# Kernel optimization log

Hardware: AMD Instinct MI355X
Metric: run time of the kernel (lower is better)

Reference implementation:

```python
import jax, jax.numpy as jnp
import numpy as np

B, C, L = 8, 256, 2048      # batch, res_channels, seq_len
E = 2 * C                    # attention / S4 width = 512
CH = 4                       # S4 channels
SQRT_HALF = 0.7071067811865476


def setup_inputs() -> dict:
    key = jax.random.key(0)
    ks = jax.random.split(key, 12)
    def n(k, s, sc):
        return jax.random.normal(k, s, dtype=jnp.float32) * sc
    return dict(
        x=jax.random.normal(ks[0], (B, C, L), dtype=jnp.float32),
        original=jax.random.normal(ks[1], (B, C, L), dtype=jnp.float32),
        sn_scale=jnp.ones((1, C, 1), jnp.float32),
        conv_w=n(ks[2], (E, C, 3), 0.05), conv_b=jnp.zeros((E,), jnp.float32),
        s4_ln_g=jnp.ones((E,), jnp.float32), s4_ln_b=jnp.zeros((E,), jnp.float32),
        s4_kernel=n(ks[3], (CH, E, L), 0.01),           # long-conv kernel per channel
        s4_D=n(ks[4], (CH, E), 1.0),                     # skip connection D
        s4_out_w=n(ks[5], (E, CH * E), 0.02), s4_out_b=jnp.zeros((E,), jnp.float32),
        attn_v_w=n(ks[6], (E, E), 0.02), attn_v_b=jnp.zeros((E,), jnp.float32),
        attn_o_w=n(ks[7], (E, E), 0.02), attn_o_b=jnp.zeros((E,), jnp.float32),
        res_w=n(ks[8], (C, C, 1), 0.05), res_b=jnp.zeros((C,), jnp.float32),
        skip_w=n(ks[9], (C, C, 1), 0.05), skip_b=jnp.zeros((C,), jnp.float32),
    )


def reference(x, original, sn_scale, conv_w, conv_b, s4_ln_g, s4_ln_b,
              s4_kernel, s4_D, s4_out_w, s4_out_b,
              attn_v_w, attn_v_b, attn_o_w, attn_o_b,
              res_w, res_b, skip_w, skip_b):
    eps = 1e-8
    # RMSNorm over channel dim (dim=1)
    rms = jnp.sqrt(jnp.sum(x * x, axis=1, keepdims=True)) / np.sqrt(x.shape[1]).astype(np.float32)
    x_n = sn_scale * x / (rms + eps)
    # h = x + original (pre-norm x), conv k=3 pad=1, GELU
    h = x + original
    h = jax.lax.conv_general_dilated(h, conv_w, (1,), [(1, 1)],
                                     dimension_numbers=('NCH', 'OIH', 'NCH'))
    h = jax.nn.gelu(h + conv_b[None, :, None], approximate=False)
    # --- S4 / GConv: LN over channels, FFT causal long conv, D-skip, GELU, out linear ---
    mu = h.mean(axis=1, keepdims=True)
    var = h.var(axis=1, keepdims=True)
    u = (h - mu) / jnp.sqrt(var + 1e-5) * s4_ln_g[None, :, None] + s4_ln_b[None, :, None]
    n2 = 2 * u.shape[-1]
    uf = jnp.fft.rfft(u, n=n2)                      # (B, E, F)
    kf = jnp.fft.rfft(s4_kernel, n=n2)              # (CH, E, F)
    y = jnp.fft.irfft(jnp.einsum('bhf,chf->bchf', uf, kf), n=n2)[..., :u.shape[-1]]
    y = y + s4_D[None, :, :, None] * u[:, None]     # (B, CH, E, L)
    y = jax.nn.gelu(y.reshape(y.shape[0], CH * E, y.shape[-1]), approximate=False)
    h_t = jnp.einsum('oc,bcl->bol', s4_out_w, y) + s4_out_b[None, :, None]  # (B, E, L)
    # --- local-window MHA with window_size=1: each position attends only to itself,
    # softmax over a single unmasked score == 1, so out = Wo @ (Wv @ x + bv) + bo exactly ---
    v = jnp.einsum('oe,bel->bol', attn_v_w, h_t) + attn_v_b[None, :, None]
    h_s = jnp.einsum('oe,bel->bol', attn_o_w, v) + attn_o_b[None, :, None]
    h2 = h_t + h_s
    out = jnp.tanh(h2[:, :C]) * jax.nn.sigmoid(h2[:, C:])
    res = jnp.einsum('oc,bcl->bol', res_w[:, :, 0], out) + res_b[None, :, None]
    skip = jnp.einsum('oc,bcl->bol', skip_w[:, :, 0], out) + skip_b[None, :, None]
    return ((x_n + res) * SQRT_HALF, skip)
```

## Files before the change

kernel.cpp:

```cpp
#include <hip/hip_runtime.h>
#include <hip/hip_bf16.h>
#include <math.h>

typedef __attribute__((ext_vector_type(8))) short short8;
typedef __attribute__((ext_vector_type(4))) float float4_t;
typedef __attribute__((ext_vector_type(2))) float cf2;
typedef unsigned short ushort_t;
typedef unsigned int uint_t;

#define NBL 16384

#define WS_CONVA   ((size_t)0)
#define WS_WV      ((size_t)786432)
#define WS_WO      ((size_t)1310720)
#define WS_W1      ((size_t)1835008)
#define WS_WCAT    ((size_t)3932160)
#define WS_A2      ((size_t)4194304)
#define WS_ACOMB   ((size_t)4718592)
#define WS_BCOMB   ((size_t)6815744)
#define WS_XN      ((size_t)6819840)
#define WS_H0PT    ((size_t)23597056)
#define WS_U       ((size_t)31993856)
#define WS_GT      ((size_t)65548288)
#define WS_UF      WS_GT
#define WS_KF      ((size_t)99102720)
#define WS_G       ((size_t)132657152)
#define WS_GATET   (WS_G + 25165824)
#define WS_UB      ((size_t)208162816)

__device__ __forceinline__ float gelu_f(float x) {
    float t = x * x;
    float a2 = x * fmaf(0.07135481627f, t, 1.59576912161f);
    return x / (1.f + __expf(-a2));
}
__device__ __forceinline__ float tanh_f(float a) {
    return 1.f - 2.f / (1.f + __expf(2.f * a));
}
__device__ __forceinline__ float sigmoid_f(float b) {
    return 1.f / (1.f + __expf(-b));
}

__device__ __forceinline__ unsigned int pack_bf2(float a, float b) {
#if __has_builtin(__builtin_amdgcn_cvt_pk_bf16_f32)
    auto v = __builtin_amdgcn_cvt_pk_bf16_f32(a, b);
    unsigned int r; __builtin_memcpy(&r, &v, 4); return r;
#else
    __hip_bfloat16 ha = __float2bfloat16(a), hb = __float2bfloat16(b);
    unsigned short ua = *(unsigned short*)&ha, ub = *(unsigned short*)&hb;
    return (unsigned int)ua | ((unsigned int)ub << 16);
#endif
}
__device__ __forceinline__ ushort_t f2bfu(float a) {
    __hip_bfloat16 h = __float2bfloat16(a);
    return *(ushort_t*)&h;
}
__device__ __forceinline__ cf2 unpack_c(unsigned int v) {
    cf2 r;
    r.x = __uint_as_float(v << 16);
    r.y = __uint_as_float(v & 0xffff0000u);
    return r;
}
__device__ __forceinline__ float bf2f(ushort_t u) {
    return __uint_as_float(((unsigned int)u) << 16);
}

__device__ __forceinline__ void cp16(const ushort_t* g, ushort_t* l) {
    __builtin_amdgcn_global_load_lds(
        (__attribute__((address_space(1))) void*)(void*)g,
        (__attribute__((address_space(3))) void*)l, 16, 0, 0);
}

__device__ __forceinline__ cf2 cswap(cf2 a) { return __builtin_shufflevector(a, a, 1, 0); }
template<int SGN>
__device__ __forceinline__ cf2 cmuli(cf2 a) {
    cf2 s = cswap(a);
    return s * cf2{(float)(-SGN), (float)SGN};
}
__device__ __forceinline__ cf2 cmul(cf2 a, cf2 b) {
    cf2 t = cswap(a) * cf2{-b.y, b.y};
    return a * cf2{b.x, b.x} + t;
}
__device__ __forceinline__ cf2 cmulc(cf2 a, float wr, float wi) {
    cf2 t = cswap(a) * cf2{-wi, wi};
    return a * cf2{wr, wr} + t;
}

__global__ __launch_bounds__(256) void wprep_kernel(
    const float* __restrict__ conv_w, const float* __restrict__ attn_v_w,
    const float* __restrict__ attn_o_w, const float* __restrict__ s4_out_w,
    const float* __restrict__ res_w, const float* __restrict__ skip_w,
    __hip_bfloat16* __restrict__ convA, __hip_bfloat16* __restrict__ WvT,
    __hip_bfloat16* __restrict__ WoBf, __hip_bfloat16* __restrict__ W1T,
    __hip_bfloat16* __restrict__ Wcat)
{
    const int N0 = 393216, N1 = 655360, N2c = 917504, N3 = 1966080, N4 = 2097152;
    for (int i = blockIdx.x * 256 + threadIdx.x; i < N4; i += gridDim.x * 256) {
        if (i < N0) {
            int m = i / 768, r = i - m * 768, dk = r >> 8, c = r & 255;
            convA[i] = __float2bfloat16(conv_w[m * 768 + c * 3 + dk]);
        } else if (i < N1) {
            int j = i - N0; int row = j >> 9, e = j & 511;
            WvT[j] = __float2bfloat16(attn_v_w[e * 512 + row]);
        } else if (i < N2c) {
            WoBf[i - N1] = __float2bfloat16(attn_o_w[i - N1]);
        } else if (i < N3) {
            int j = i - N2c; int ck = j >> 9, e = j & 511;
            W1T[j] = __float2bfloat16(s4_out_w[e * 2048 + ck]);
        } else {
            int j = i - N3; int m = j >> 8, c = j & 255;
            float v = (m < 256) ? res_w[m * 256 + c] : skip_w[(m - 256) * 256 + c];
            Wcat[j] = __float2bfloat16(v);
        }
    }
}

__global__ __launch_bounds__(256) void bias2_kernel(
    const __hip_bfloat16* __restrict__ A2, const float* __restrict__ s4_out_b,
    const float* __restrict__ attn_o_w, const float* __restrict__ attn_v_b,
    const float* __restrict__ attn_o_b, float* __restrict__ bcomb)
{
    __shared__ float red[256];
    int o = blockIdx.x, t = threadIdx.x;
    float s = 0.f;
    for (int e = t; e < 512; e += 256)
        s += __bfloat162float(A2[o * 512 + e]) * s4_out_b[e] + attn_o_w[o * 512 + e] * attn_v_b[e];
    red[t] = s; __syncthreads();
    for (int k = 128; k > 0; k >>= 1) { if (t < k) red[t] += red[t + k]; __syncthreads(); }
    if (t == 0) bcomb[o] = red[0] + attn_o_b[o];
}

__global__ __launch_bounds__(512) void prep_kernel(
    const float* __restrict__ x, const float* __restrict__ orig,
    const float* __restrict__ sn, ushort_t* __restrict__ xnb, ushort_t* __restrict__ h0pT)
{
    __shared__ float red[8][64];
    __shared__ ushort_t T[256 * 66];
    int blk = blockIdx.x, t = threadIdx.x;
    int lane = t & 63, cg = t >> 6;
    int b = blk >> 5, l0 = (blk & 31) << 6;
    size_t basein = (size_t)b * 524288 + l0 + lane;
    float ss = 0.f;
    for (int c = cg; c < 256; c += 8) {
        size_t idx = basein + (size_t)c * 2048;
        float xv = x[idx], ov = orig[idx];
        ss += xv * xv;
        T[c * 66 + lane] = f2bfu(xv + ov);
    }
    red[cg][lane] = ss;
    __syncthreads();
    float tot = 0.f;
    #pragma unroll
    for (int k = 0; k < 8; ++k) tot += red[k][lane];
    float inv = 1.0f / (sqrtf(tot) * 0.0625f + 1e-8f);
    __hip_bfloat16* xo = (__hip_bfloat16*)xnb;
    for (int c = cg; c < 256; c += 8) {
        size_t idx = basein + (size_t)c * 2048;
        xo[idx] = __float2bfloat16(sn[c] * x[idx] * inv);
    }
    int c2 = t & 255, half = t >> 8;
    size_t rowbase = (size_t)(b * 2050 + 1 + l0);
    for (int r = half; r < 64; r += 2)
        h0pT[(rowbase + r) * 256 + c2] = T[c2 * 66 + r];
    if ((blk & 31) == 0) {
        if (t < 256) h0pT[(size_t)(b * 2050) * 256 + t] = 0;
        else         h0pT[(size_t)(b * 2050 + 2049) * 256 + (t - 256)] = 0;
    }
}

__global__ __launch_bounds__(512) void ln_kernel(
    const ushort_t* __restrict__ h, ushort_t* __restrict__ ub,
    const float* __restrict__ gam, const float* __restrict__ bet)
{
    __shared__ float r1[8][64], r2[8][64];
    int blk = blockIdx.x, t = threadIdx.x;
    int lane = t & 63, og = t >> 6;
    int n = (blk << 6) + lane;
    float s1 = 0.f, s2 = 0.f;
    for (int o = og; o < 512; o += 8) { float v = bf2f(h[(size_t)o * NBL + n]); s1 += v; s2 += v * v; }
    r1[og][lane] = s1; r2[og][lane] = s2;
    __syncthreads();
    float mu = 0.f, m2 = 0.f;
    #pragma unroll
    for (int k = 0; k < 8; ++k) { mu += r1[k][lane]; m2 += r2[k][lane]; }
    mu *= (1.f / 512.f); m2 *= (1.f / 512.f);
    float rstd = rsqrtf(m2 - mu * mu + 1e-5f);
    int b = n >> 11, l = n & 2047;
    size_t sbase = (size_t)(b >> 1) * 4096 + 2 * l + (b & 1);
    for (int o = og; o < 512; o += 8) {
        size_t idx = (size_t)o * NBL + n;
        ub[(size_t)o * 16384 + sbase] = f2bfu((bf2f(h[idx]) - mu) * rstd * gam[o] + bet[o]);
    }
}

#define PERM(m) ((((m) & 3) << 2) | ((m) >> 2))

template<int SGN>
__device__ __forceinline__ void dft4p(cf2& a0, cf2& a1, cf2& a2, cf2& a3) {
    cf2 t0 = a0 + a2, t1 = a0 - a2, t2 = a1 + a3, t3 = a1 - a3;
    cf2 j3 = cmuli<SGN>(t3);
    a0 = t0 + t2; a2 = t0 - t2;
    a1 = t1 + j3; a3 = t1 - j3;
}
template<int SGN>
__device__ __forceinline__ void dft4p_half(cf2& a0, cf2& a1, cf2& a2, cf2& a3) {
    cf2 u0 = a0, u1 = a1;
    cf2 j1 = cmuli<SGN>(u1);
    a0 = u0 + u1; a2 = u0 - u1;
    a1 = u0 + j1; a3 = u0 - j1;
}
template<int SGN>
__device__ __forceinline__ void dft4p_out01(cf2 a0, cf2 a1, cf2 a2, cf2 a3, cf2& o0, cf2& o1) {
    cf2 t0 = a0 + a2, t1 = a0 - a2, t2 = a1 + a3, t3 = a1 - a3;
    o0 = t0 + t2;
    o1 = t1 + cmuli<SGN>(t3);
}

template<int SGN>
__device__ __forceinline__ void dft16_stepB(cf2* x) {
    const float sg = (float)SGN;
    const float C16[10] = {1.f, 0.92387953f, 0.70710678f, 0.38268343f, 0.f,
                           -0.38268343f, -0.70710678f, -0.92387953f, -1.f, -0.92387953f};
    const float S16[10] = {0.f, 0.38268343f, 0.70710678f, 0.92387953f, 1.f,
                           0.92387953f, 0.70710678f, 0.38268343f, 0.f, -0.38268343f};
    #pragma unroll
    for (int s = 1; s < 4; ++s)
        #pragma unroll
        for (int r = 1; r < 4; ++r) {
            int e = s * r;
            x[4 * s + r] = cmulc(x[4 * s + r], C16[e], sg * S16[e]);
        }
}
template<int SGN>
__device__ __forceinline__ void dft16p(cf2* x) {
    #pragma unroll
    for (int r = 0; r < 4; ++r) dft4p<SGN>(x[r], x[4 + r], x[8 + r], x[12 + r]);
    dft16_stepB<SGN>(x);
    #pragma unroll
    for (int s = 0; s < 4; ++s) dft4p<SGN>(x[4 * s], x[4 * s + 1], x[4 * s + 2], x[4 * s + 3]);
}
template<int SGN>
__device__ __forceinline__ void dft16_halfin(cf2* x) {
    #pragma unroll
    for (int r = 0; r < 4; ++r) dft4p_half<SGN>(x[r], x[4 + r], x[8 + r], x[12 + r]);
    dft16_stepB<SGN>(x);
    #pragma unroll
    for (int s = 0; s < 4; ++s) dft4p<SGN>(x[4 * s], x[4 * s + 1], x[4 * s + 2], x[4 * s + 3]);
}
template<int SGN>
__device__ __forceinline__ void dft16_halfout(cf2* x, cf2* y) {
    #pragma unroll
    for (int r = 0; r < 4; ++r) dft4p<SGN>(x[r], x[4 + r], x[8 + r], x[12 + r]);
    dft16_stepB<SGN>(x);
    #pragma unroll
    for (int s = 0; s < 4; ++s)
        dft4p_out01<SGN>(x[4 * s], x[4 * s + 1], x[4 * s + 2], x[4 * s + 3], y[s], y[4 + s]);
}

template<int SGN>
__device__ __forceinline__ void tw_after(cf2* x, float p, float invQ) {
    float s1, c1; __sincosf((float)SGN * 6.283185307179586f * p * invQ, &s1, &c1);
    cf2 w1 = {c1, s1}, w = w1;
    #pragma unroll
    for (int m = 1; m < 16; ++m) { x[PERM(m)] = cmul(x[PERM(m)], w); w = cmul(w, w1); }
}
template<int SGN>
__device__ __forceinline__ void tw_before(cf2* x, float p, float invQ) {
    float s1, c1; __sincosf((float)SGN * 6.283185307179586f * p * invQ, &s1, &c1);
    cf2 w1 = {c1, s1}, w = w1;
    #pragma unroll
    for (int j = 1; j < 16; ++j) { x[j] = cmul(x[j], w); w = cmul(w, w1); }
}

__global__ __launch_bounds__(256) void fft_fwd_kernel(
    const ushort_t* __restrict__ ubf, const float* __restrict__ s4k,
    uint4* __restrict__ uf, uint4* __restrict__ kf)
{
    __shared__ cf2 S[4368];
    int wg = blockIdx.x, t = threadIdx.x;
    cf2 x[16];
    if (wg < 2048) {
        int bp = wg >> 9, e = wg & 511;
        const unsigned int* p0 = (const unsigned int*)ubf + (size_t)e * 8192 + (size_t)bp * 2048;
        #pragma unroll
        for (int j = 0; j < 8; ++j) x[j] = unpack_c(p0[j * 256 + t]);
    } else {
        const float* p0 = s4k + (size_t)(wg - 2048) * 2048;
        #pragma unroll
        for (int j = 0; j < 8; ++j) x[j] = cf2{p0[j * 256 + t], 0.f};
    }
    dft16_halfin<-1>(x);
    tw_after<-1>(x, (float)t, 1.f / 4096.f);
    int tb = 17 * (t >> 4) + (t & 15);
    #pragma unroll
    for (int m = 0; m < 16; ++m) S[tb + 273 * m] = x[PERM(m)];
    __syncthreads();
    int b2 = 273 * (t >> 4) + (t & 15);
    #pragma unroll
    for (int j = 0; j < 16; ++j) x[j] = S[b2 + 17 * j];
    dft16p<-1>(x);
    tw_after<-1>(x, (float)(t & 15), 1.f / 256.f);
    #pragma unroll
    for (int m = 0; m < 16; ++m) S[b2 + 17 * m] = x[PERM(m)];
    __syncthreads();
    int b3 = 273 * (t >> 4) + 17 * (t & 15);
    #pragma unroll
    for (int j = 0; j < 16; ++j) x[j] = S[b3 + j];
    dft16p<-1>(x);
    const float sc = (wg < 2048) ? 1.f : (1.f / 4096.f);
    uint4* dst = ((wg < 2048) ? (uf + (size_t)wg * 1024) : (kf + (size_t)(wg - 2048) * 1024)) + 4 * t;
    #pragma unroll
    for (int q = 0; q < 4; ++q) {
        uint4 o;
        cf2 v0 = x[PERM(4 * q)] * sc, v1 = x[PERM(4 * q + 1)] * sc;
        cf2 v2 = x[PERM(4 * q + 2)] * sc, v3 = x[PERM(4 * q + 3)] * sc;
        o.x = pack_bf2(v0.x, v0.y);
        o.y = pack_bf2(v1.x, v1.y);
        o.z = pack_bf2(v2.x, v2.y);
        o.w = pack_bf2(v3.x, v3.y);
        dst[q] = o;
    }
}

__global__ __launch_bounds__(256) void fft_inv_kernel(
    const uint4* __restrict__ uf, const uint4* __restrict__ kf,
    unsigned int* __restrict__ g2)
{
    __shared__ cf2 S[4368];
    int wg = blockIdx.x, t = threadIdx.x;
    int bp = wg >> 11, ch = (wg >> 9) & 3, e = wg & 511;
    const uint4* zr = uf + (size_t)(bp * 512 + e) * 1024 + 4 * t;
    const uint4* kr = kf + (size_t)(ch * 512 + e) * 1024 + 4 * t;
    cf2 x[16];
    #pragma unroll
    for (int q = 0; q < 4; ++q) {
        uint4 a4 = zr[q], b4 = kr[q];
        x[4 * q + 0] = cmul(unpack_c(a4.x), unpack_c(b4.x));
        x[4 * q + 1] = cmul(unpack_c(a4.y), unpack_c(b4.y));
        x[4 * q + 2] = cmul(unpack_c(a4.z), unpack_c(b4.z));
        x[4 * q + 3] = cmul(unpack_c(a4.w), unpack_c(b4.w));
    }
    dft16p<1>(x);
    int b1 = 273 * (t >> 4) + 17 * (t & 15);
    #pragma unroll
    for (int m = 0; m < 16; ++m) S[b1 + m] = x[PERM(m)];
    __syncthreads();
    int b2 = 273 * (t >> 4) + (t & 15);
    #pragma unroll
    for (int j = 0; j < 16; ++j) x[j] = S[b2 + 17 * j];
    tw_before<1>(x, (float)(t & 15), 1.f / 256.f);
    dft16p<1>(x);
    #pragma unroll
    for (int m = 0; m < 16; ++m) S[b2 + 17 * m] = x[PERM(m)];
    __syncthreads();
    int b3 = 17 * (t >> 4) + (t & 15);
    #pragma unroll
    for (int j = 0; j < 16; ++j) x[j] = S[b3 + 273 * j];
    tw_before<1>(x, (float)t, 1.f / 4096.f);
    cf2 y[8];
    dft16_halfout<1>(x, y);
    unsigned int* go = g2 + (size_t)(ch * 512 + e) * 8192 + (size_t)bp * 2048;
    #pragma unroll
    for (int m = 0; m < 8; ++m)
        go[m * 256 + t] = pack_bf2(y[m].x, y[m].y);
}

__global__ __launch_bounds__(256) void gdt_kernel(
    const unsigned int* __restrict__ g2, const unsigned int* __restrict__ ub2,
    const float* __restrict__ s4D, ushort_t* __restrict__ gT)
{
    __shared__ unsigned int S2[64 * 65];
    int c0 = blockIdx.x * 64, r0 = blockIdx.y * 64;
    int t = threadIdx.x, lx = t & 63, ly0 = t >> 6;
    #pragma unroll
    for (int ly = ly0; ly < 64; ly += 4) {
        int r = r0 + ly, cp = c0 + lx;
        cf2 y2 = unpack_c(g2[(size_t)r * 8192 + cp]);
        cf2 u2 = unpack_c(ub2[(size_t)(r & 511) * 8192 + cp]);
        float d = s4D[r];
        float v0 = gelu_f(fmaf(d, u2.x, y2.x));
        float v1 = gelu_f(fmaf(d, u2.y, y2.y));
        S2[ly * 65 + lx] = pack_bf2(v0, v1);
    }
    __syncthreads();
    #pragma unroll
    for (int ly = ly0; ly < 64; ly += 4) {
        int oc = c0 + ly;
        unsigned int v = S2[lx * 65 + ly];
        int bp = oc >> 11, l = oc & 2047;
        size_t na = (size_t)(bp * 4096 + l) * 2048 + r0 + lx;
        gT[na] = (ushort_t)(v & 0xffff);
        gT[na + 4194304] = (ushort_t)(v >> 16);
    }
}

template<int BSRC, int EPI>
__global__ __launch_bounds__(256) void gemm_kernel(
    const ushort_t* __restrict__ A, const ushort_t* __restrict__ Bm,
    ushort_t* __restrict__ Cb, float* __restrict__ Cf,
    int M, int N, int K,
    const float* __restrict__ bias, const float* __restrict__ bias2,
    const ushort_t* __restrict__ xnb, float* __restrict__ dout)
{
    __shared__ ushort_t SM[8704];
    ushort_t* Alds = SM;
    ushort_t* Blds = SM + 4096;
    const int t = threadIdx.x;
    const int n0 = blockIdx.x * 128, m0 = blockIdx.y * 128;
    const int w = t >> 6, lane = t & 63, quad = lane >> 4, lr = lane & 15;
    const int wm = (w >> 1) * 64, wn = (w & 1) * 64;

    const int r0q = w * 32 + (lane >> 2);
    const int slot = lane & 3;
    int ar0 = m0 + r0q, ar1 = m0 + r0q + 16;
    if (EPI == 5) {
        ar0 = (r0q < 64) ? (64 * blockIdx.y + r0q) : (192 + 64 * blockIdx.y + r0q);
        int r1 = r0q + 16;
        ar1 = (r1 < 64) ? (64 * blockIdx.y + r1) : (192 + 64 * blockIdx.y + r1);
    }
    const ushort_t* aSrc0 = A + (size_t)ar0 * K + slot * 8;
    const ushort_t* aSrc1 = A + (size_t)ar1 * K + slot * 8;
    const ushort_t* bSrc0;
    const ushort_t* bSrc1;
    if (BSRC == 0) {
        bSrc0 = Bm + (size_t)(n0 + r0q) * K + slot * 8;
        bSrc1 = Bm + (size_t)(n0 + r0q + 16) * K + slot * 8;
    } else {
        int nn0 = n0 + r0q, nn1 = nn0 + 16;
        bSrc0 = Bm + (size_t)((nn0 >> 11) * 2050 + (nn0 & 2047)) * 256 + slot * 8;
        bSrc1 = Bm + (size_t)((nn1 >> 11) * 2050 + (nn1 & 2047)) * 256 + slot * 8;
    }
    ushort_t* aD0 = Alds + w * 1024;
    ushort_t* aD1 = Alds + w * 1024 + 512;
    ushort_t* bD0 = Blds + w * 1024;
    ushort_t* bD1 = Blds + w * 1024 + 512;

    float4_t acc[4][4];
    #pragma unroll
    for (int i = 0; i < 4; ++i)
        #pragma unroll
        for (int j = 0; j < 4; ++j) { float4_t z = {0.f, 0.f, 0.f, 0.f}; acc[i][j] = z; }

    for (int kt = 0; kt < K; kt += 32) {
        if (kt) __syncthreads();
        cp16(aSrc0 + kt, aD0);
        cp16(aSrc1 + kt, aD1);
        if (BSRC == 0) {
            cp16(bSrc0 + kt, bD0);
            cp16(bSrc1 + kt, bD1);
        } else {
            int boff = (kt >> 8) * 256 + (kt & 255);
            cp16(bSrc0 + boff, bD0);
            cp16(bSrc1 + boff, bD1);
        }
        __syncthreads();
        short8 af[4], bfr[4];
        #pragma unroll
        for (int im = 0; im < 4; ++im)
            af[im] = *(const short8*)&Alds[(wm + im * 16 + lr) * 32 + quad * 8];
        #pragma unroll
        for (int in_ = 0; in_ < 4; ++in_)
            bfr[in_] = *(const short8*)&Blds[(wn + in_ * 16 + lr) * 32 + quad * 8];
        #pragma unroll
        for (int im = 0; im < 4; ++im)
            #pragma unroll
            for (int in_ = 0; in_ < 4; ++in_)
                acc[im][in_] = __builtin_amdgcn_mfma_f32_16x16x32_bf16(af[im], bfr[in_], acc[im][in_], 0, 0, 0);
    }

    if (EPI == 5) {
        const int by = blockIdx.y;
        __syncthreads();
        #pragma unroll
        for (int p = 0; p < 2; ++p) {
            if (p) __syncthreads();
            if ((w & 1) == p) {
                #pragma unroll
                for (int im = 0; im < 4; ++im)
                    #pragma unroll
                    for (int in_ = 0; in_ < 4; ++in_) {
                        int nl = in_ * 16 + lr;
                        #pragma unroll
                        for (int r = 0; r < 4; ++r) {
                            int i = wm + im * 16 + quad * 4 + r;
                            int me = (i < 64) ? (64 * by + i) : (192 + 64 * by + i);
                            SM[i * 68 + nl] = f2bfu(acc[im][in_][r] + bias[me]);
                        }
                    }
            }
            __syncthreads();
            int nl = t >> 2, gcb = (t & 3) * 16;
            size_t obase = (size_t)(n0 + 64 * p + nl) * 256 + 64 * by + gcb;
            short8 o0, o1;
            #pragma unroll
            for (int j = 0; j < 16; ++j) {
                int gc = gcb + j;
                float a = bf2f(SM[gc * 68 + nl]);
                float bb = bf2f(SM[(gc + 64) * 68 + nl]);
                ushort_t gv = f2bfu(tanh_f(a) * sigmoid_f(bb));
                if (j < 8) o0[j] = (short)gv; else o1[j - 8] = (short)gv;
            }
            *(short8*)(Cb + obase) = o0;
            *(short8*)(Cb + obase + 8) = o1;
        }
        return;
    }

    #pragma unroll
    for (int im = 0; im < 4; ++im) {
        #pragma unroll
        for (int in_ = 0; in_ < 4; ++in_) {
            int n = n0 + wn + in_ * 16 + lr;
            int mb = m0 + wm + im * 16 + quad * 4;
            #pragma unroll
            for (int r = 0; r < 4; ++r) {
                int m = mb + r;
                float v = acc[im][in_][r];
                if (EPI == 0) {
                    v += bias[m];
                    ((__hip_bfloat16*)Cb)[(size_t)m * N + n] = __float2bfloat16(gelu_f(v));
                } else if (EPI == 1) {
                    v += (m == n) ? 1.0f : 0.0f;
                    ((__hip_bfloat16*)Cb)[(size_t)m * N + n] = __float2bfloat16(v);
                } else if (EPI == 2) {
                    ((__hip_bfloat16*)Cb)[(size_t)m * N + n] = __float2bfloat16(v);
                } else {
                    int bb = n >> 11, ll = n & 2047;
                    if (m < 256) {
                        v += bias[m];
                        int idx = (bb << 19) + (m << 11) + ll;
                        dout[idx] = (bf2f(xnb[idx]) + v) * 0.70710678118654752f;
                    } else {
                        v += bias2[m - 256];
                        dout[4194304 + (bb << 19) + ((m - 256) << 11) + ll] = v;
                    }
                }
            }
        }
    }
}

extern "C" void kernel_launch(void* const* d_in, const int* in_sizes, int n_in,
                              void* d_out, int out_size, void* d_ws, size_t ws_size,
                              hipStream_t stream)
{
    const float* x         = (const float*)d_in[0];
    const float* original  = (const float*)d_in[1];
    const float* sn_scale  = (const float*)d_in[2];
    const float* conv_w    = (const float*)d_in[3];
    const float* conv_b    = (const float*)d_in[4];
    const float* s4_ln_g   = (const float*)d_in[5];
    const float* s4_ln_b   = (const float*)d_in[6];
    const float* s4_kernel = (const float*)d_in[7];
    const float* s4_D      = (const float*)d_in[8];
    const float* s4_out_w  = (const float*)d_in[9];
    const float* s4_out_b  = (const float*)d_in[10];
    const float* attn_v_w  = (const float*)d_in[11];
    const float* attn_v_b  = (const float*)d_in[12];
    const float* attn_o_w  = (const float*)d_in[13];
    const float* attn_o_b  = (const float*)d_in[14];
    const float* res_w     = (const float*)d_in[15];
    const float* res_b     = (const float*)d_in[16];
    const float* skip_w    = (const float*)d_in[17];
    const float* skip_b    = (const float*)d_in[18];

    char* ws = (char*)d_ws;
    __hip_bfloat16* convA = (__hip_bfloat16*)(ws + WS_CONVA);
    __hip_bfloat16* WvT   = (__hip_bfloat16*)(ws + WS_WV);
    __hip_bfloat16* WoBf  = (__hip_bfloat16*)(ws + WS_WO);
    __hip_bfloat16* W1T   = (__hip_bfloat16*)(ws + WS_W1);
    __hip_bfloat16* Wcat  = (__hip_bfloat16*)(ws + WS_WCAT);
    ushort_t* A2    = (ushort_t*)(ws + WS_A2);
    ushort_t* Acomb = (ushort_t*)(ws + WS_ACOMB);
    float* bcombp  = (float*)(ws + WS_BCOMB);
    ushort_t* xnb  = (ushort_t*)(ws + WS_XN);
    ushort_t* h0pT = (ushort_t*)(ws + WS_H0PT);
    ushort_t* hP   = (ushort_t*)(ws + WS_U);
    ushort_t* ubP  = (ushort_t*)(ws + WS_UB);
    uint4* ufP = (uint4*)(ws + WS_UF);
    uint4* kfP = (uint4*)(ws + WS_KF);
    unsigned int* g2P = (unsigned int*)(ws + WS_G);
    ushort_t* gT    = (ushort_t*)(ws + WS_GT);
    ushort_t* gateT = (ushort_t*)(ws + WS_GATET);

    wprep_kernel<<<dim3(4096), dim3(256), 0, stream>>>(conv_w, attn_v_w, attn_o_w, s4_out_w,
        res_w, skip_w, convA, WvT, WoBf, W1T, Wcat);
    gemm_kernel<0, 1><<<dim3(4, 4), dim3(256), 0, stream>>>(
        (const ushort_t*)WoBf, (const ushort_t*)WvT, A2, nullptr, 512, 512, 512,
        nullptr, nullptr, nullptr, nullptr);
    bias2_kernel<<<dim3(512), dim3(256), 0, stream>>>(
        (const __hip_bfloat16*)A2, s4_out_b, attn_o_w, attn_v_b, attn_o_b, bcombp);
    gemm_kernel<0, 2><<<dim3(16, 4), dim3(256), 0, stream>>>(
        A2, (const ushort_t*)W1T, Acomb, nullptr, 512, 2048, 512,
        nullptr, nullptr, nullptr, nullptr);

    prep_kernel<<<dim3(256), dim3(512), 0, stream>>>(x, original, sn_scale, xnb, h0pT);
    gemm_kernel<1, 0><<<dim3(128, 4), dim3(256), 0, stream>>>(
        (const ushort_t*)convA, h0pT, hP, nullptr, 512, NBL, 768,
        conv_b, nullptr, nullptr, nullptr);
    ln_kernel<<<dim3(256), dim3(512), 0, stream>>>(hP, ubP, s4_ln_g, s4_ln_b);
    fft_fwd_kernel<<<dim3(4096), dim3(256), 0, stream>>>(ubP, s4_kernel, ufP, kfP);
    fft_inv_kernel<<<dim3(8192), dim3(256), 0, stream>>>(ufP, kfP, g2P);
    gdt_kernel<<<dim3(128, 32), dim3(256), 0, stream>>>(
        g2P, (const unsigned int*)ubP, s4_D, gT);
    gemm_kernel<0, 5><<<dim3(128, 4), dim3(256), 0, stream>>>(
        (const ushort_t*)Acomb, gT, gateT, nullptr, 512, NBL, 2048,
        bcombp, nullptr, nullptr, nullptr);
    gemm_kernel<0, 4><<<dim3(128, 4), dim3(256), 0, stream>>>(
        (const ushort_t*)Wcat, gateT, nullptr, nullptr, 512, NBL, 256,
        res_b, skip_b, xnb, (float*)d_out);
}
```

Baseline: 430.2 us.

## Double-buffer LDS tiles in GEMM kernel to overlap loads with MFMA

The GEMM main loop now uses two LDS buffers. The next K-slice is prefetched with cp16 while MFMAs run on the current buffer, leaving one barrier per iteration instead of two. This is meant to hide global-to-LDS latency behind compute. Shared memory grows from about 17 KB to 32 KB per block, which may lower occupancy. Correctness also depends on cp16's completion semantics relative to the single barrier.

```diff
diff --git a/kernel.cpp b/kernel.cpp
--- a/kernel.cpp
+++ b/kernel.cpp
@@ -401,9 +401,7 @@
     const float* __restrict__ bias, const float* __restrict__ bias2,
     const ushort_t* __restrict__ xnb, float* __restrict__ dout)
 {
-    __shared__ ushort_t SM[8704];
-    ushort_t* Alds = SM;
-    ushort_t* Blds = SM + 4096;
+    __shared__ ushort_t SM[16384];
     const int t = threadIdx.x;
     const int n0 = blockIdx.x * 128, m0 = blockIdx.y * 128;
     const int w = t >> 6, lane = t & 63, quad = lane >> 4, lr = lane & 15;
@@ -429,10 +427,8 @@
         bSrc0 = Bm + (size_t)((nn0 >> 11) * 2050 + (nn0 & 2047)) * 256 + slot * 8;
         bSrc1 = Bm + (size_t)((nn1 >> 11) * 2050 + (nn1 & 2047)) * 256 + slot * 8;
     }
-    ushort_t* aD0 = Alds + w * 1024;
-    ushort_t* aD1 = Alds + w * 1024 + 512;
-    ushort_t* bD0 = Blds + w * 1024;
-    ushort_t* bD1 = Blds + w * 1024 + 512;
+    const int aOff = w * 1024;
+    const int bOff = 4096 + w * 1024;
 
     float4_t acc[4][4];
     #pragma unroll
@@ -440,19 +436,29 @@
         #pragma unroll
         for (int j = 0; j < 4; ++j) { float4_t z = {0.f, 0.f, 0.f, 0.f}; acc[i][j] = z; }
 
-    for (int kt = 0; kt < K; kt += 32) {
-        if (kt) __syncthreads();
-        cp16(aSrc0 + kt, aD0);
-        cp16(aSrc1 + kt, aD1);
-        if (BSRC == 0) {
-            cp16(bSrc0 + kt, bD0);
-            cp16(bSrc1 + kt, bD1);
-        } else {
-            int boff = (kt >> 8) * 256 + (kt & 255);
-            cp16(bSrc0 + boff, bD0);
-            cp16(bSrc1 + boff, bD1);
+    cp16(aSrc0, SM + aOff);
+    cp16(aSrc1, SM + aOff + 512);
+    cp16(bSrc0, SM + bOff);
+    cp16(bSrc1, SM + bOff + 512);
+    __syncthreads();
+
+    for (int kt = 0, cb = 0; kt < K; kt += 32, cb ^= 8192) {
+        int kn = kt + 32;
+        if (kn < K) {
+            int nb = cb ^ 8192;
+            cp16(aSrc0 + kn, SM + nb + aOff);
+            cp16(aSrc1 + kn, SM + nb + aOff + 512);
+            if (BSRC == 0) {
+                cp16(bSrc0 + kn, SM + nb + bOff);
+                cp16(bSrc1 + kn, SM + nb + bOff + 512);
+            } else {
+                int boff = (kn >> 8) * 256 + (kn & 255);
+                cp16(bSrc0 + boff, SM + nb + bOff);
+                cp16(bSrc1 + boff, SM + nb + bOff + 512);
+            }
         }
-        __syncthreads();
+        const ushort_t* Alds = SM + cb;
+        const ushort_t* Blds = SM + cb + 4096;
         short8 af[4], bfr[4];
         #pragma unroll
         for (int im = 0; im < 4; ++im)
@@ -465,11 +471,11 @@
             #pragma unroll
             for (int in_ = 0; in_ < 4; ++in_)
                 acc[im][in_] = __builtin_amdgcn_mfma_f32_16x16x32_bf16(af[im], bfr[in_], acc[im][in_], 0, 0, 0);
+        __syncthreads();
     }
 
     if (EPI == 5) {
         const int by = blockIdx.y;
-        __syncthreads();
         #pragma unroll
         for (int p = 0; p < 2; ++p) {
             if (p) __syncthreads();
```

Result: faster. 413.0 us (-4.0%).

## Double-buffer GEMM LDS tiles, swizzle layout, and halve N tile to 64

Applied to the files above, without the earlier changes.

Rewrites the shared bf16 MFMA GEMM so that global-to-LDS copies for the next 32-wide K slice are issued into a second LDS buffer while the current slice is computed. This removes one barrier per K step and overlaps loads with math. It also XOR-swizzles the LDS column slot to cut bank conflicts, and shrinks the block tile from 128x128 to 128x64, which doubles the grid sizes and adds occupancy hints through launch bounds. In exchange each block reuses less of the A tile and uses twice the shared memory.

```diff
diff --git a/kernel.cpp b/kernel.cpp
--- a/kernel.cpp
+++ b/kernel.cpp
@@ -394,121 +394,120 @@
 }
 
 template<int BSRC, int EPI>
-__global__ __launch_bounds__(256) void gemm_kernel(
+__global__ __launch_bounds__(256, 4) void gemm_kernel(
     const ushort_t* __restrict__ A, const ushort_t* __restrict__ Bm,
     ushort_t* __restrict__ Cb, float* __restrict__ Cf,
     int M, int N, int K,
     const float* __restrict__ bias, const float* __restrict__ bias2,
     const ushort_t* __restrict__ xnb, float* __restrict__ dout)
 {
-    __shared__ ushort_t SM[8704];
-    ushort_t* Alds = SM;
-    ushort_t* Blds = SM + 4096;
+    __shared__ ushort_t SM[16384];
     const int t = threadIdx.x;
-    const int n0 = blockIdx.x * 128, m0 = blockIdx.y * 128;
+    const int n0 = blockIdx.x * 64, m0 = blockIdx.y * 128;
     const int w = t >> 6, lane = t & 63, quad = lane >> 4, lr = lane & 15;
-    const int wm = (w >> 1) * 64, wn = (w & 1) * 64;
-
-    const int r0q = w * 32 + (lane >> 2);
-    const int slot = lane & 3;
+    const int wm = (w >> 1) * 64, wn = (w & 1) * 32;
+
+    const int srow = lane >> 2;
+    const int swslot = ((lane & 3) ^ ((lane >> 3) & 3)) * 8;
+    const int r0q = w * 32 + srow;
     int ar0 = m0 + r0q, ar1 = m0 + r0q + 16;
     if (EPI == 5) {
         ar0 = (r0q < 64) ? (64 * blockIdx.y + r0q) : (192 + 64 * blockIdx.y + r0q);
         int r1 = r0q + 16;
         ar1 = (r1 < 64) ? (64 * blockIdx.y + r1) : (192 + 64 * blockIdx.y + r1);
     }
-    const ushort_t* aSrc0 = A + (size_t)ar0 * K + slot * 8;
-    const ushort_t* aSrc1 = A + (size_t)ar1 * K + slot * 8;
-    const ushort_t* bSrc0;
-    const ushort_t* bSrc1;
-    if (BSRC == 0) {
-        bSrc0 = Bm + (size_t)(n0 + r0q) * K + slot * 8;
-        bSrc1 = Bm + (size_t)(n0 + r0q + 16) * K + slot * 8;
-    } else {
-        int nn0 = n0 + r0q, nn1 = nn0 + 16;
-        bSrc0 = Bm + (size_t)((nn0 >> 11) * 2050 + (nn0 & 2047)) * 256 + slot * 8;
-        bSrc1 = Bm + (size_t)((nn1 >> 11) * 2050 + (nn1 & 2047)) * 256 + slot * 8;
-    }
-    ushort_t* aD0 = Alds + w * 1024;
-    ushort_t* aD1 = Alds + w * 1024 + 512;
-    ushort_t* bD0 = Blds + w * 1024;
-    ushort_t* bD1 = Blds + w * 1024 + 512;
-
-    float4_t acc[4][4];
+    const ushort_t* aSrc0 = A + (size_t)ar0 * K + swslot;
+    const ushort_t* aSrc1 = A + (size_t)ar1 * K + swslot;
+    const int nrow = n0 + w * 16 + srow;
+    const ushort_t* bSrc;
+    if (BSRC == 0) bSrc = Bm + (size_t)nrow * K + swslot;
+    else           bSrc = Bm + (size_t)((nrow >> 11) * 2050 + (nrow & 2047)) * 256 + swslot;
+
+    const int aD = w * 1024;
+    const int bD = 4096 + w * 512;
+
+    float4_t acc[4][2];
     #pragma unroll
     for (int i = 0; i < 4; ++i)
         #pragma unroll
-        for (int j = 0; j < 4; ++j) { float4_t z = {0.f, 0.f, 0.f, 0.f}; acc[i][j] = z; }
-
-    for (int kt = 0; kt < K; kt += 32) {
-        if (kt) __syncthreads();
-        cp16(aSrc0 + kt, aD0);
-        cp16(aSrc1 + kt, aD1);
-        if (BSRC == 0) {
-            cp16(bSrc0 + kt, bD0);
-            cp16(bSrc1 + kt, bD1);
-        } else {
-            int boff = (kt >> 8) * 256 + (kt & 255);
-            cp16(bSrc0 + boff, bD0);
-            cp16(bSrc1 + boff, bD1);
-        }
+        for (int j = 0; j < 2; ++j) { float4_t z = {0.f, 0.f, 0.f, 0.f}; acc[i][j] = z; }
+
+    const int qsw = (quad ^ ((lr >> 1) & 3)) << 3;
+
+#define STAGE(BUF, KK) do {                                                     \
+        cp16(aSrc0 + (KK), SM + (BUF) + aD);                                    \
+        cp16(aSrc1 + (KK), SM + (BUF) + aD + 512);                              \
+        if (BSRC == 0) cp16(bSrc + (KK), SM + (BUF) + bD);                      \
+        else cp16(bSrc + (((KK) >> 8) * 256 + ((KK) & 255)), SM + (BUF) + bD);  \
+    } while (0)
+
+#define COMPUTE(BUF) do {                                                       \
+        const ushort_t* Al = SM + (BUF);                                        \
+        const ushort_t* Bl = SM + (BUF) + 4096;                                 \
+        short8 af[4], bfr[2];                                                   \
+        _Pragma("unroll")                                                       \
+        for (int im = 0; im < 4; ++im)                                          \
+            af[im] = *(const short8*)&Al[(wm + im * 16 + lr) * 32 + qsw];       \
+        _Pragma("unroll")                                                       \
+        for (int in_ = 0; in_ < 2; ++in_)                                       \
+            bfr[in_] = *(const short8*)&Bl[(wn + in_ * 16 + lr) * 32 + qsw];    \
+        _Pragma("unroll")                                                       \
+        for (int im = 0; im < 4; ++im)                                          \
+            _Pragma("unroll")                                                   \
+            for (int in_ = 0; in_ < 2; ++in_)                                   \
+                acc[im][in_] = __builtin_amdgcn_mfma_f32_16x16x32_bf16(         \
+                    af[im], bfr[in_], acc[im][in_], 0, 0, 0);                   \
+    } while (0)
+
+    STAGE(0, 0);
+    __syncthreads();
+
+    for (int kt = 0; kt < K; kt += 64) {
+        STAGE(8192, kt + 32);
+        COMPUTE(0);
         __syncthreads();
-        short8 af[4], bfr[4];
-        #pragma unroll
-        for (int im = 0; im < 4; ++im)
-            af[im] = *(const short8*)&Alds[(wm + im * 16 + lr) * 32 + quad * 8];
-        #pragma unroll
-        for (int in_ = 0; in_ < 4; ++in_)
-            bfr[in_] = *(const short8*)&Blds[(wn + in_ * 16 + lr) * 32 + quad * 8];
+        if (kt + 64 < K) STAGE(0, kt + 64);
+        COMPUTE(8192);
+        __syncthreads();
+    }
+#undef STAGE
+#undef COMPUTE
+
+    if (EPI == 5) {
+        const int by = blockIdx.y;
         #pragma unroll
         for (int im = 0; im < 4; ++im)
             #pragma unroll
-            for (int in_ = 0; in_ < 4; ++in_)
-                acc[im][in_] = __builtin_amdgcn_mfma_f32_16x16x32_bf16(af[im], bfr[in_], acc[im][in_], 0, 0, 0);
-    }
-
-    if (EPI == 5) {
-        const int by = blockIdx.y;
+            for (int in_ = 0; in_ < 2; ++in_) {
+                int nl = wn + in_ * 16 + lr;
+                #pragma unroll
+                for (int r = 0; r < 4; ++r) {
+                    int i = wm + im * 16 + quad * 4 + r;
+                    int me = (i < 64) ? (64 * by + i) : (192 + 64 * by + i);
+                    SM[i * 68 + nl] = f2bfu(acc[im][in_][r] + bias[me]);
+                }
+            }
         __syncthreads();
+        int nl = t >> 2, gcb = (t & 3) * 16;
+        size_t obase = (size_t)(n0 + nl) * 256 + 64 * by + gcb;
+        short8 o0, o1;
         #pragma unroll
-        for (int p = 0; p < 2; ++p) {
-            if (p) __syncthreads();
-            if ((w & 1) == p) {
-                #pragma unroll
-                for (int im = 0; im < 4; ++im)
-                    #pragma unroll
-                    for (int in_ = 0; in_ < 4; ++in_) {
-                        int nl = in_ * 16 + lr;
-                        #pragma unroll
-                        for (int r = 0; r < 4; ++r) {
-                            int i = wm + im * 16 + quad * 4 + r;
-                            int me = (i < 64) ? (64 * by + i) : (192 + 64 * by + i);
-                            SM[i * 68 + nl] = f2bfu(acc[im][in_][r] + bias[me]);
-                        }
-                    }
-            }
-            __syncthreads();
-            int nl = t >> 2, gcb = (t & 3) * 16;
-            size_t obase = (size_t)(n0 + 64 * p + nl) * 256 + 64 * by + gcb;
-            short8 o0, o1;
-            #pragma unroll
-            for (int j = 0; j < 16; ++j) {
-                int gc = gcb + j;
-                float a = bf2f(SM[gc * 68 + nl]);
-                float bb = bf2f(SM[(gc + 64) * 68 + nl]);
-                ushort_t gv = f2bfu(tanh_f(a) * sigmoid_f(bb));
-                if (j < 8) o0[j] = (short)gv; else o1[j - 8] = (short)gv;
-            }
-            *(short8*)(Cb + obase) = o0;
-            *(short8*)(Cb + obase + 8) = o1;
+        for (int j = 0; j < 16; ++j) {
+            int gc = gcb + j;
+            float a = bf2f(SM[gc * 68 + nl]);
+            float bb = bf2f(SM[(gc + 64) * 68 + nl]);
+            ushort_t gv = f2bfu(tanh_f(a) * sigmoid_f(bb));
+            if (j < 8) o0[j] = (short)gv; else o1[j - 8] = (short)gv;
         }
+        *(short8*)(Cb + obase) = o0;
+        *(short8*)(Cb + obase + 8) = o1;
         return;
     }
 
     #pragma unroll
     for (int im = 0; im < 4; ++im) {
         #pragma unroll
-        for (int in_ = 0; in_ < 4; ++in_) {
+        for (int in_ = 0; in_ < 2; ++in_) {
             int n = n0 + wn + in_ * 16 + lr;
             int mb = m0 + wm + im * 16 + quad * 4;
             #pragma unroll
@@ -584,17 +583,17 @@
 
     wprep_kernel<<<dim3(4096), dim3(256), 0, stream>>>(conv_w, attn_v_w, attn_o_w, s4_out_w,
         res_w, skip_w, convA, WvT, WoBf, W1T, Wcat);
-    gemm_kernel<0, 1><<<dim3(4, 4), dim3(256), 0, stream>>>(
+    gemm_kernel<0, 1><<<dim3(8, 4), dim3(256), 0, stream>>>(
         (const ushort_t*)WoBf, (const ushort_t*)WvT, A2, nullptr, 512, 512, 512,
         nullptr, nullptr, nullptr, nullptr);
     bias2_kernel<<<dim3(512), dim3(256), 0, stream>>>(
         (const __hip_bfloat16*)A2, s4_out_b, attn_o_w, attn_v_b, attn_o_b, bcombp);
-    gemm_kernel<0, 2><<<dim3(16, 4), dim3(256), 0, stream>>>(
+    gemm_kernel<0, 2><<<dim3(32, 4), dim3(256), 0, stream>>>(
         A2, (const ushort_t*)W1T, Acomb, nullptr, 512, 2048, 512,
         nullptr, nullptr, nullptr, nullptr);
 
     prep_kernel<<<dim3(256), dim3(512), 0, stream>>>(x, original, sn_scale, xnb, h0pT);
-    gemm_kernel<1, 0><<<dim3(128, 4), dim3(256), 0, stream>>>(
+    gemm_kernel<1, 0><<<dim3(256, 4), dim3(256), 0, stream>>>(
         (const ushort_t*)convA, h0pT, hP, nullptr, 512, NBL, 768,
         conv_b, nullptr, nullptr, nullptr);
     ln_kernel<<<dim3(256), dim3(512), 0, stream>>>(hP, ubP, s4_ln_g, s4_ln_b);
@@ -602,10 +601,10 @@
     fft_inv_kernel<<<dim3(8192), dim3(256), 0, stream>>>(ufP, kfP, g2P);
     gdt_kernel<<<dim3(128, 32), dim3(256), 0, stream>>>(
         g2P, (const unsigned int*)ubP, s4_D, gT);
-    gemm_kernel<0, 5><<<dim3(128, 4), dim3(256), 0, stream>>>(
+    gemm_kernel<0, 5><<<dim3(256, 4), dim3(256), 0, stream>>>(
         (const ushort_t*)Acomb, gT, gateT, nullptr, 512, NBL, 2048,
         bcombp, nullptr, nullptr, nullptr);
-    gemm_kernel<0, 4><<<dim3(128, 4), dim3(256), 0, stream>>>(
+    gemm_kernel<0, 4><<<dim3(256, 4), dim3(256), 0, stream>>>(
         (const ushort_t*)Wcat, gateT, nullptr, nullptr, 512, NBL, 256,
         res_b, skip_b, xnb, (float*)d_out);
 }
```

Result: faster. 406.5 us (-5.5%).
